# Performance work log

Measured on AMD Instinct MI355X. Metric: run time of the kernel, lower is better.

The kernel has to match this reference:

```python
import jax, jax.numpy as jnp
import numpy as np

DIM = 256; HEADS = 8; WSIZES = (8, 16); SHIFTS = (4, 8); H = 64; W = 64
NG = len(WSIZES)          # n_group
CH = DIM // NG            # channel per group = 128
GH = HEADS // NG          # gnum_heads = 4
GC = CH // GH             # gchannel (head dim) = 32
M = NG; D_SK = CH // 2    # SKConv: M groups, d = channel//r (r=2)


def _rel_pos_index(ws):
    coords = np.stack(np.meshgrid(np.arange(ws), np.arange(ws), indexing='ij'))
    cf = coords.reshape(2, -1)
    rel = (cf[:, :, None] - cf[:, None, :]).transpose(1, 2, 0).copy()
    rel[:, :, 0] += ws - 1
    rel[:, :, 1] += ws - 1
    rel[:, :, 0] *= 2 * ws - 1
    return rel.sum(-1)  # (ws*ws, ws*ws) int


def _attn_mask(ws, shift, Hp, Wp):
    img = np.zeros((Hp, Wp))
    sl = (slice(0, -ws), slice(-ws, -shift), slice(-shift, None))
    cnt = 0
    for hs in sl:
        for wsl in sl:
            img[hs, wsl] = cnt; cnt += 1
    mw = img.reshape(Hp // ws, ws, Wp // ws, ws).transpose(0, 2, 1, 3).reshape(-1, ws * ws)
    am = mw[:, None, :] - mw[:, :, None]  # unsqueeze(1) - unsqueeze(2)
    return np.where(am != 0, -100.0, 0.0).astype(np.float32)  # (nW, N, N)


def _part(x, ws):  # (B,H,W,C) -> (B*nW, ws, ws, C)
    B, Hx, Wx, C = x.shape
    x = x.reshape(B, Hx // ws, ws, Wx // ws, ws, C).transpose(0, 1, 3, 2, 4, 5)
    return x.reshape(-1, ws, ws, C)


def _reverse(win, ws, Hx, Wx, B):  # (B*nW, ws, ws, C) -> (B,H,W,C)
    C = win.shape[-1]
    x = win.reshape(B, Hx // ws, Wx // ws, ws, ws, C).transpose(0, 1, 3, 2, 4, 5)
    return x.reshape(B, Hx, Wx, C)


def _gelu(x):
    return jax.nn.gelu(x, approximate=False)  # torch nn.GELU default


def _skconv(x, pw, pb, f1w, f1b, f2w, f2b, phw, phb):
    bs, Hx, Wx, _ = x.shape
    # split channels into M groups of CH
    input_groups = x.transpose(0, 3, 1, 2).reshape(bs, M, CH, Hx, Wx)
    feats = x.reshape(bs, Hx * Wx, DIM) @ pw + pb
    feats_proj = feats.transpose(0, 2, 1).reshape(bs, DIM, Hx, Wx)
    fa = _gelu(feats).transpose(0, 2, 1).reshape(bs, DIM, Hx, Wx)
    feats_S = fa.mean(axis=(2, 3))                       # GAP -> (bs, DIM)
    z = _gelu(feats_S @ f1w + f1b)                       # (bs, d)
    av = (z @ f2w + f2b).reshape(bs, M, CH, 1, 1)
    av = jax.nn.softmax(av, axis=1)
    feats_V = (input_groups * av).sum(axis=1)            # (bs, CH, H, W)
    feats_V = feats_V.reshape(bs, CH, Hx * Wx).transpose(0, 2, 1) @ phw + phb
    feats_V = feats_V.transpose(0, 2, 1).reshape(bs, DIM, Hx, Wx)
    return feats_proj + feats_V


def _forward(x_q, x_kv, w_q, b_q, w_kv, b_kv, rpb0, rpb1,
             sk_proj_w, sk_proj_b, sk_fc1_w, sk_fc1_b, sk_fc2_w, sk_fc2_b,
             sk_head_w, sk_head_b):
    B = x_q.shape[0]
    q = (x_q.reshape(B, -1, DIM) @ w_q + b_q).reshape(B, H, W, DIM)
    kv = x_kv.reshape(B, -1, DIM) @ w_kv + b_kv           # (B, HW, 2*DIM)
    k = kv[..., :DIM].reshape(B, H, W, DIM)
    v = kv[..., DIM:].reshape(B, H, W, DIM)
    rpbs = (rpb0, rpb1)
    outs = []
    for i, (ws, sh) in enumerate(zip(WSIZES, SHIFTS)):
        qg = q[..., i * CH:(i + 1) * CH]
        kg = k[..., i * CH:(i + 1) * CH]
        vg = v[..., i * CH:(i + 1) * CH]
        if sh > 0:
            qg = jnp.roll(qg, (-sh, -sh), (1, 2))
            kg = jnp.roll(kg, (-sh, -sh), (1, 2))
            vg = jnp.roll(vg, (-sh, -sh), (1, 2))
        N = ws * ws
        qw = _part(qg, ws).reshape(-1, N, GH, GC).transpose(0, 2, 1, 3)  # (B_,GH,N,GC)
        kw = _part(kg, ws).reshape(-1, N, GH, GC).transpose(0, 2, 1, 3)
        vw = _part(vg, ws).reshape(-1, N, GH, GC).transpose(0, 2, 1, 3)
        scale = GC ** -0.5
        attn = jnp.einsum('bhnd,bhmd->bhnm', qw * scale, kw)
        idx = _rel_pos_index(ws).reshape(-1)
        bias = rpbs[i][idx].reshape(N, N, GH).transpose(2, 0, 1)         # (GH,N,N)
        attn = attn + bias[None]
        if sh > 0:
            mask = jnp.asarray(_attn_mask(ws, sh, H, W))                 # (nW,N,N)
            nW = mask.shape[0]
            attn = attn.reshape(-1, nW, GH, N, N) + mask[None, :, None]
            attn = attn.reshape(-1, GH, N, N)
        attn = jax.nn.softmax(attn, axis=-1)
        xw = jnp.einsum('bhnm,bhmd->bhnd', attn, vw)
        xw = xw.transpose(0, 2, 1, 3).reshape(-1, ws, ws, CH)
        xg = _reverse(xw, ws, H, W, B)
        if sh > 0:
            xg = jnp.roll(xg, (sh, sh), (1, 2))
        outs.append(xg)
    x = jnp.concatenate(outs, axis=-1)                    # (B,H,W,DIM)
    return _skconv(x, sk_proj_w, sk_proj_b, sk_fc1_w, sk_fc1_b,
                   sk_fc2_w, sk_fc2_b, sk_head_w, sk_head_b)


def setup_inputs() -> dict:
    key = jax.random.key(0)
    ks = jax.random.split(key, 16)
    B = 16
    s = lambda n: 1.0 / np.sqrt(n)
    return {
        'x_q': jax.random.normal(ks[0], (B, H, W, DIM), jnp.float32),
        'x_kv': jax.random.normal(ks[1], (B, H, W, DIM), jnp.float32),
        'w_q': jax.random.normal(ks[2], (DIM, DIM), jnp.float32) * s(DIM),
        'b_q': jnp.zeros((DIM,), jnp.float32),
        'w_kv': jax.random.normal(ks[3], (DIM, 2 * DIM), jnp.float32) * s(DIM),
        'b_kv': jnp.zeros((2 * DIM,), jnp.float32),
        'rpb0': jax.random.normal(ks[4], ((2 * WSIZES[0] - 1) ** 2, GH), jnp.float32) * 0.02,
        'rpb1': jax.random.normal(ks[5], ((2 * WSIZES[1] - 1) ** 2, GH), jnp.float32) * 0.02,
        'sk_proj_w': jax.random.normal(ks[6], (DIM, DIM), jnp.float32) * s(DIM),
        'sk_proj_b': jnp.zeros((DIM,), jnp.float32),
        'sk_fc1_w': jax.random.normal(ks[7], (DIM, D_SK), jnp.float32) * s(DIM),
        'sk_fc1_b': jnp.zeros((D_SK,), jnp.float32),
        'sk_fc2_w': jax.random.normal(ks[8], (D_SK, M * CH), jnp.float32) * s(D_SK),
        'sk_fc2_b': jnp.zeros((M * CH,), jnp.float32),
        'sk_head_w': jax.random.normal(ks[9], (CH, DIM), jnp.float32) * s(CH),
        'sk_head_b': jnp.zeros((DIM,), jnp.float32),
    }


def reference(x_q, x_kv, w_q, b_q, w_kv, b_kv, rpb0, rpb1,
              sk_proj_w, sk_proj_b, sk_fc1_w, sk_fc1_b, sk_fc2_w, sk_fc2_b,
              sk_head_w, sk_head_b):
    return _forward(x_q, x_kv, w_q, b_q, w_kv, b_kv, rpb0, rpb1,
                    sk_proj_w, sk_proj_b, sk_fc1_w, sk_fc1_b, sk_fc2_w, sk_fc2_b,
                    sk_head_w, sk_head_b)
```

## Files before the change

### kernel.cpp

```cpp
#include <hip/hip_runtime.h>
#include <cstddef>
#include <cstdint>


typedef __attribute__((ext_vector_type(8))) short short8v;
typedef __attribute__((ext_vector_type(4))) short short4v;
typedef __attribute__((ext_vector_type(4))) float f32x4;

__device__ __forceinline__ float gelu_f(float x) {
  return 0.5f * x * (1.0f + erff(x * 0.7071067811865475f));
}

__device__ __forceinline__ unsigned short f32_to_bf16_rne(float f) {
  unsigned u = __float_as_uint(f);
  unsigned r = 0x7FFFu + ((u >> 16) & 1u);
  return (unsigned short)((u + r) >> 16);
}
__device__ __forceinline__ float bf16_hi_to_f32(unsigned short h) {
  return __uint_as_float(((unsigned)h) << 16);
}

__global__ void decomp_w(const float* __restrict__ W,
                         unsigned short* __restrict__ hiT,
                         unsigned short* __restrict__ loT, int N, int K)
{
  const int k = blockIdx.y;
  const int n = blockIdx.x * 64 + threadIdx.x;
  const float f = W[(size_t)k * N + n];
  const unsigned short h = f32_to_bf16_rne(f);
  const unsigned short l = f32_to_bf16_rne(f - bf16_hi_to_f32(h));
  hiT[(size_t)n * K + k] = h;
  loT[(size_t)n * K + k] = l;
}

__global__ __launch_bounds__(512) void gemm_mfma_bias(
    const float* __restrict__ A, const unsigned short* __restrict__ WhT,
    const unsigned short* __restrict__ WlT, const float* __restrict__ bias,
    float* __restrict__ C, int N)
{
  constexpr int K = 256;
  __shared__ alignas(16) unsigned short Ah[4096];
  __shared__ alignas(16) unsigned short Al[4096];
  __shared__ alignas(16) unsigned short Bh[8192];
  __shared__ alignas(16) unsigned short Bl[8192];

  const int row0 = blockIdx.x * 128;
  const int col0 = blockIdx.y * 256;
  const int tid = threadIdx.x;
  const int lane = tid & 63;
  const int wave = tid >> 6;
  const int wm = wave >> 2, wn = wave & 3;

  f32x4 acc[4][4];
#pragma unroll
  for (int mi = 0; mi < 4; ++mi)
#pragma unroll
    for (int ni = 0; ni < 4; ++ni) {
      f32x4 z = {0.f, 0.f, 0.f, 0.f};
      acc[mi][ni] = z;
    }

  float4 pa[2];
  short8v pbh[2], pbl[2];

#define LOAD_TILE_QKV(k0_)                                                     \
  {                                                                            \
    _Pragma("unroll") for (int p = 0; p < 2; ++p) {                            \
      int flat = p * 512 + tid;                                                \
      int m = flat >> 3, kq = flat & 7;                                        \
      pa[p] = *(const float4*)(A + (size_t)(row0 + m) * K + (k0_) + kq * 4);   \
    }                                                                          \
    _Pragma("unroll") for (int p = 0; p < 2; ++p) {                            \
      int flat = p * 512 + tid;                                                \
      int n = flat >> 2, ko = flat & 3;                                        \
      const size_t off = (size_t)(col0 + n) * 256 + (k0_) + ko * 8;            \
      pbh[p] = *(const short8v*)(WhT + off);                                   \
      pbl[p] = *(const short8v*)(WlT + off);                                   \
    }                                                                          \
  }

  LOAD_TILE_QKV(0);

  for (int ks = 0; ks < 8; ++ks) {
    __syncthreads();
#pragma unroll
    for (int p = 0; p < 2; ++p) {
      int flat = p * 512 + tid;
      int m = flat >> 3, kq = flat & 7;
      float fx[4] = {pa[p].x, pa[p].y, pa[p].z, pa[p].w};
      unsigned short h[4], l[4];
#pragma unroll
      for (int j = 0; j < 4; ++j) {
        h[j] = f32_to_bf16_rne(fx[j]);
        l[j] = f32_to_bf16_rne(fx[j] - bf16_hi_to_f32(h[j]));
      }
      int e4 = (m >> 4) * 512 + (kq >> 1) * 128 + (m & 15) * 8 + (kq & 1) * 4;
      short4v hv = {(short)h[0], (short)h[1], (short)h[2], (short)h[3]};
      short4v lv = {(short)l[0], (short)l[1], (short)l[2], (short)l[3]};
      *(short4v*)&Ah[e4] = hv;
      *(short4v*)&Al[e4] = lv;
    }
#pragma unroll
    for (int p = 0; p < 2; ++p) {
      int flat = p * 512 + tid;
      int n = flat >> 2, ko = flat & 3;
      int e = (n >> 4) * 512 + ko * 128 + (n & 15) * 8;
      *(short8v*)&Bh[e] = pbh[p];
      *(short8v*)&Bl[e] = pbl[p];
    }
    __syncthreads();

    if (ks < 7) LOAD_TILE_QKV((ks + 1) * 32);

    short8v ah[4], alo[4], bh[4], blo[4];
#pragma unroll
    for (int mi = 0; mi < 4; ++mi) {
      int base = (wm * 4 + mi) * 512 + lane * 8;
      ah[mi] = *(const short8v*)&Ah[base];
      alo[mi] = *(const short8v*)&Al[base];
    }
#pragma unroll
    for (int ni = 0; ni < 4; ++ni) {
      int base = (wn * 4 + ni) * 512 + lane * 8;
      bh[ni] = *(const short8v*)&Bh[base];
      blo[ni] = *(const short8v*)&Bl[base];
    }
#pragma unroll
    for (int mi = 0; mi < 4; ++mi)
#pragma unroll
      for (int ni = 0; ni < 4; ++ni) {
        acc[mi][ni] = __builtin_amdgcn_mfma_f32_16x16x32_bf16(ah[mi], bh[ni], acc[mi][ni], 0, 0, 0);
        acc[mi][ni] = __builtin_amdgcn_mfma_f32_16x16x32_bf16(ah[mi], blo[ni], acc[mi][ni], 0, 0, 0);
        acc[mi][ni] = __builtin_amdgcn_mfma_f32_16x16x32_bf16(alo[mi], bh[ni], acc[mi][ni], 0, 0, 0);
      }
  }
#undef LOAD_TILE_QKV

#pragma unroll
  for (int mi = 0; mi < 4; ++mi) {
    const int rowb = row0 + wm * 64 + mi * 16 + (lane >> 4) * 4;
#pragma unroll
    for (int ni = 0; ni < 4; ++ni) {
      const int col = col0 + wn * 64 + ni * 16 + (lane & 15);
      const float bv = bias[col];
#pragma unroll
      for (int r = 0; r < 4; ++r)
        C[(size_t)(rowb + r) * N + col] = acc[mi][ni][r] + bv;
    }
  }
}

__global__ __launch_bounds__(512) void gemm_mfma_proj(
    const float* __restrict__ Act, const unsigned short* __restrict__ WhT,
    const unsigned short* __restrict__ WlT, const float* __restrict__ bias,
    float* __restrict__ featsT, float* __restrict__ part)
{
  __shared__ alignas(16) unsigned short Wh[4096];
  __shared__ alignas(16) unsigned short Wl[4096];
  __shared__ alignas(16) unsigned short Bh[8192];
  __shared__ alignas(16) unsigned short Bl[8192];
  __shared__ float pgelu[4][128];

  const int hw0 = blockIdx.x * 256;
  const int c0 = blockIdx.y * 128;
  const int b = hw0 >> 12;
  const int hwp0 = hw0 & 4095;
  const int tid = threadIdx.x;
  const int lane = tid & 63;
  const int wave = tid >> 6;
  const int wc = wave >> 2, wh = wave & 3;

  f32x4 acc[4][4];
#pragma unroll
  for (int mi = 0; mi < 4; ++mi)
#pragma unroll
    for (int ni = 0; ni < 4; ++ni) {
      f32x4 z = {0.f, 0.f, 0.f, 0.f};
      acc[mi][ni] = z;
    }

  float4 pact[4];
  short8v pwh, pwl;

#define LOAD_TILE_PROJ(k0_)                                                    \
  {                                                                            \
    _Pragma("unroll") for (int p = 0; p < 4; ++p) {                            \
      int f = p * 512 + tid;                                                   \
      int h = f >> 3, kq = f & 7;                                              \
      pact[p] = *(const float4*)(Act + (size_t)(hw0 + h) * 256 + (k0_) + kq * 4); \
    }                                                                          \
    {                                                                          \
      int c = tid >> 2, ko = tid & 3;                                          \
      const size_t off = (size_t)(c0 + c) * 256 + (k0_) + ko * 8;              \
      pwh = *(const short8v*)(WhT + off);                                      \
      pwl = *(const short8v*)(WlT + off);                                      \
    }                                                                          \
  }

  LOAD_TILE_PROJ(0);

  for (int ks = 0; ks < 8; ++ks) {
    __syncthreads();
    {
      int c = tid >> 2, ko = tid & 3;
      int e = (c >> 4) * 512 + ko * 128 + (c & 15) * 8;
      *(short8v*)&Wh[e] = pwh;
      *(short8v*)&Wl[e] = pwl;
    }
#pragma unroll
    for (int p = 0; p < 4; ++p) {
      int f = p * 512 + tid;
      int h = f >> 3, kq = f & 7;
      float fx[4] = {pact[p].x, pact[p].y, pact[p].z, pact[p].w};
      unsigned short hh[4], ll[4];
#pragma unroll
      for (int j = 0; j < 4; ++j) {
        hh[j] = f32_to_bf16_rne(fx[j]);
        ll[j] = f32_to_bf16_rne(fx[j] - bf16_hi_to_f32(hh[j]));
      }
      int e4 = (h >> 4) * 512 + (kq >> 1) * 128 + (h & 15) * 8 + (kq & 1) * 4;
      short4v hv = {(short)hh[0], (short)hh[1], (short)hh[2], (short)hh[3]};
      short4v lv = {(short)ll[0], (short)ll[1], (short)ll[2], (short)ll[3]};
      *(short4v*)&Bh[e4] = hv;
      *(short4v*)&Bl[e4] = lv;
    }
    __syncthreads();

    if (ks < 7) LOAD_TILE_PROJ((ks + 1) * 32);

    short8v wfh[4], wfl[4], bfh[4], bfl[4];
#pragma unroll
    for (int mi = 0; mi < 4; ++mi) {
      int base = (wc * 4 + mi) * 512 + lane * 8;
      wfh[mi] = *(const short8v*)&Wh[base];
      wfl[mi] = *(const short8v*)&Wl[base];
    }
#pragma unroll
    for (int ni = 0; ni < 4; ++ni) {
      int base = (wh * 4 + ni) * 512 + lane * 8;
      bfh[ni] = *(const short8v*)&Bh[base];
      bfl[ni] = *(const short8v*)&Bl[base];
    }
#pragma unroll
    for (int mi = 0; mi < 4; ++mi)
#pragma unroll
      for (int ni = 0; ni < 4; ++ni) {
        acc[mi][ni] = __builtin_amdgcn_mfma_f32_16x16x32_bf16(wfh[mi], bfh[ni], acc[mi][ni], 0, 0, 0);
        acc[mi][ni] = __builtin_amdgcn_mfma_f32_16x16x32_bf16(wfh[mi], bfl[ni], acc[mi][ni], 0, 0, 0);
        acc[mi][ni] = __builtin_amdgcn_mfma_f32_16x16x32_bf16(wfl[mi], bfh[ni], acc[mi][ni], 0, 0, 0);
      }
  }
#undef LOAD_TILE_PROJ

  float gsum[4][4];
#pragma unroll
  for (int mi = 0; mi < 4; ++mi)
#pragma unroll
    for (int r = 0; r < 4; ++r) gsum[mi][r] = 0.f;

#pragma unroll
  for (int mi = 0; mi < 4; ++mi) {
    const int c = c0 + wc * 64 + mi * 16 + (lane >> 4) * 4;
#pragma unroll
    for (int ni = 0; ni < 4; ++ni) {
      const int hwl = wh * 64 + ni * 16 + (lane & 15);
      const size_t base = ((size_t)b * 256 + c) * 4096 + hwp0 + hwl;
#pragma unroll
      for (int r = 0; r < 4; ++r) {
        const float val = acc[mi][ni][r] + bias[c + r];
        featsT[base + (size_t)r * 4096] = val;
        gsum[mi][r] += gelu_f(val);
      }
    }
  }
#pragma unroll
  for (int mi = 0; mi < 4; ++mi)
#pragma unroll
    for (int r = 0; r < 4; ++r) {
      float s = gsum[mi][r];
      s += __shfl_xor(s, 1);
      s += __shfl_xor(s, 2);
      s += __shfl_xor(s, 4);
      s += __shfl_xor(s, 8);
      gsum[mi][r] = s;
    }
  if ((lane & 15) == 0) {
#pragma unroll
    for (int mi = 0; mi < 4; ++mi)
#pragma unroll
      for (int r = 0; r < 4; ++r)
        pgelu[wh][wc * 64 + mi * 16 + (lane >> 4) * 4 + r] = gsum[mi][r];
  }
  __syncthreads();
  if (tid < 128) {
    const float s = pgelu[0][tid] + pgelu[1][tid] + pgelu[2][tid] + pgelu[3][tid];
    const int rbl = hwp0 >> 8;
    part[((size_t)b * 16 + rbl) * 256 + c0 + tid] = s;
  }
}

__global__ __launch_bounds__(512) void gemm_mfma_final(
    const float* __restrict__ Act, const float* __restrict__ featsT,
    const float* __restrict__ av, const unsigned short* __restrict__ WhT,
    const unsigned short* __restrict__ WlT, const float* __restrict__ bias,
    float* __restrict__ out)
{
  __shared__ alignas(16) unsigned short Wh[4096];
  __shared__ alignas(16) unsigned short Wl[4096];
  __shared__ alignas(16) unsigned short Bh[8192];
  __shared__ alignas(16) unsigned short Bl[8192];
  __shared__ float avs[256];

  const int hw0 = blockIdx.x * 256;
  const int c0 = blockIdx.y * 128;
  const int b = hw0 >> 12;
  const int hwp0 = hw0 & 4095;
  const int tid = threadIdx.x;
  const int lane = tid & 63;
  const int wave = tid >> 6;
  const int wc = wave >> 2, wh = wave & 3;

  if (tid < 256) avs[tid] = av[b * 256 + tid];

  f32x4 acc[4][4];
#pragma unroll
  for (int mi = 0; mi < 4; ++mi)
#pragma unroll
    for (int ni = 0; ni < 4; ++ni) {
      f32x4 z = {0.f, 0.f, 0.f, 0.f};
      acc[mi][ni] = z;
    }

  float4 px[4], py[4];
  short8v pwh, pwl;

#define LOAD_TILE_FIN(k0_)                                                     \
  {                                                                            \
    _Pragma("unroll") for (int p = 0; p < 4; ++p) {                            \
      int f = p * 512 + tid;                                                   \
      int h = f >> 3, kq = f & 7;                                              \
      const float* bp = Act + (size_t)(hw0 + h) * 256 + (k0_) + kq * 4;        \
      px[p] = *(const float4*)bp;                                              \
      py[p] = *(const float4*)(bp + 128);                                      \
    }                                                                          \
    {                                                                          \
      int c = tid >> 2, ko = tid & 3;                                          \
      const size_t off = (size_t)(c0 + c) * 128 + (k0_) + ko * 8;              \
      pwh = *(const short8v*)(WhT + off);                                      \
      pwl = *(const short8v*)(WlT + off);                                      \
    }                                                                          \
  }

  LOAD_TILE_FIN(0);

  for (int ks = 0; ks < 4; ++ks) {
    const int k0 = ks * 32;
    __syncthreads();
    {
      int c = tid >> 2, ko = tid & 3;
      int e = (c >> 4) * 512 + ko * 128 + (c & 15) * 8;
      *(short8v*)&Wh[e] = pwh;
      *(short8v*)&Wl[e] = pwl;
    }
#pragma unroll
    for (int p = 0; p < 4; ++p) {
      int f = p * 512 + tid;
      int h = f >> 3, kq = f & 7;
      const float4 a0 = *(const float4*)(avs + k0 + kq * 4);
      const float4 a1 = *(const float4*)(avs + 128 + k0 + kq * 4);
      float fx[4];
      fx[0] = px[p].x * a0.x + py[p].x * a1.x;
      fx[1] = px[p].y * a0.y + py[p].y * a1.y;
      fx[2] = px[p].z * a0.z + py[p].z * a1.z;
      fx[3] = px[p].w * a0.w + py[p].w * a1.w;
      unsigned short hh[4], ll[4];
#pragma unroll
      for (int j = 0; j < 4; ++j) {
        hh[j] = f32_to_bf16_rne(fx[j]);
        ll[j] = f32_to_bf16_rne(fx[j] - bf16_hi_to_f32(hh[j]));
      }
      int e4 = (h >> 4) * 512 + (kq >> 1) * 128 + (h & 15) * 8 + (kq & 1) * 4;
      short4v hv = {(short)hh[0], (short)hh[1], (short)hh[2], (short)hh[3]};
      short4v lv = {(short)ll[0], (short)ll[1], (short)ll[2], (short)ll[3]};
      *(short4v*)&Bh[e4] = hv;
      *(short4v*)&Bl[e4] = lv;
    }
    __syncthreads();

    if (ks < 3) LOAD_TILE_FIN((ks + 1) * 32);

    short8v wfh[4], wfl[4], bfh[4], bfl[4];
#pragma unroll
    for (int mi = 0; mi < 4; ++mi) {
      int base = (wc * 4 + mi) * 512 + lane * 8;
      wfh[mi] = *(const short8v*)&Wh[base];
      wfl[mi] = *(const short8v*)&Wl[base];
    }
#pragma unroll
    for (int ni = 0; ni < 4; ++ni) {
      int base = (wh * 4 + ni) * 512 + lane * 8;
      bfh[ni] = *(const short8v*)&Bh[base];
      bfl[ni] = *(const short8v*)&Bl[base];
    }
#pragma unroll
    for (int mi = 0; mi < 4; ++mi)
#pragma unroll
      for (int ni = 0; ni < 4; ++ni) {
        acc[mi][ni] = __builtin_amdgcn_mfma_f32_16x16x32_bf16(wfh[mi], bfh[ni], acc[mi][ni], 0, 0, 0);
        acc[mi][ni] = __builtin_amdgcn_mfma_f32_16x16x32_bf16(wfh[mi], bfl[ni], acc[mi][ni], 0, 0, 0);
        acc[mi][ni] = __builtin_amdgcn_mfma_f32_16x16x32_bf16(wfl[mi], bfh[ni], acc[mi][ni], 0, 0, 0);
      }
  }
#undef LOAD_TILE_FIN

#pragma unroll
  for (int mi = 0; mi < 4; ++mi) {
    const int c = c0 + wc * 64 + mi * 16 + (lane >> 4) * 4;
#pragma unroll
    for (int ni = 0; ni < 4; ++ni) {
      const int hwl = wh * 64 + ni * 16 + (lane & 15);
      const size_t base = ((size_t)b * 256 + c) * 4096 + hwp0 + hwl;
#pragma unroll
      for (int r = 0; r < 4; ++r)
        out[base + (size_t)r * 4096] =
            acc[mi][ni][r] + bias[c + r] + featsT[base + (size_t)r * 4096];
    }
  }
}

template <int WS, int SH, int GRP>
__global__ __launch_bounds__(WS * WS) void attn_kernel(
    float* qio, const float* __restrict__ kvbuf, const float* __restrict__ rpb)
{
  constexpr int N = WS * WS;
  constexpr int NW = 64 / WS;
  constexpr int NBIAS = (2 * WS - 1) * (2 * WS - 1);
  constexpr int LOGWS = (WS == 8) ? 3 : 4;

  __shared__ float ks[N][36];
  __shared__ float vs[N][36];
  __shared__ float sbias[NBIAS];
  __shared__ int sreg[N];

  const int head = blockIdx.x & 3;
  const int win = blockIdx.x >> 2;
  const int b = win / (NW * NW);
  const int wl = win % (NW * NW);
  const int wi = wl / NW, wj = wl % NW;
  const int t = threadIdx.x;
  const int ti = t >> LOGWS, tj = t & (WS - 1);
  const int hr = wi * WS + ti, wr = wj * WS + tj;
  const int hg = (hr + SH) & 63, wg = (wr + SH) & 63;
  const int cb = GRP * 128 + head * 32;

  const size_t pos = ((size_t)b * 64 + hg) * 64 + wg;
  float* qp = qio + pos * 256 + cb;
  const float* kp = kvbuf + pos * 512 + cb;
  const float* vp = kp + 256;

  constexpr float scale = 0.17677669529663687f;
  float qreg[32];
#pragma unroll
  for (int d4 = 0; d4 < 8; ++d4) {
    float4 qv = *(const float4*)(qp + d4 * 4);
    qreg[d4 * 4 + 0] = qv.x * scale; qreg[d4 * 4 + 1] = qv.y * scale;
    qreg[d4 * 4 + 2] = qv.z * scale; qreg[d4 * 4 + 3] = qv.w * scale;
    float4 kk4 = *(const float4*)(kp + d4 * 4);
    ks[t][d4 * 4 + 0] = kk4.x; ks[t][d4 * 4 + 1] = kk4.y;
    ks[t][d4 * 4 + 2] = kk4.z; ks[t][d4 * 4 + 3] = kk4.w;
    float4 vv4 = *(const float4*)(vp + d4 * 4);
    vs[t][d4 * 4 + 0] = vv4.x; vs[t][d4 * 4 + 1] = vv4.y;
    vs[t][d4 * 4 + 2] = vv4.z; vs[t][d4 * 4 + 3] = vv4.w;
  }
  for (int i = t; i < NBIAS; i += N) sbias[i] = rpb[i * 4 + head];
  const int rrh = (hr < 64 - WS) ? 0 : ((hr < 64 - SH) ? 1 : 2);
  const int rrw = (wr < 64 - WS) ? 0 : ((wr < 64 - SH) ? 1 : 2);
  const int myreg = rrh * 3 + rrw;
  sreg[t] = myreg;
  __syncthreads();

  float oacc[32];
#pragma unroll
  for (int d = 0; d < 32; ++d) oacc[d] = 0.f;
  float mrun = -1e30f, lrun = 0.f;
  const int tbias = (ti + WS - 1) * (2 * WS - 1) + (tj + WS - 1);

  for (int mc = 0; mc < N; mc += 32) {
    float s[32];
#pragma unroll
    for (int mm = 0; mm < 32; ++mm) {
      const int m = mc + mm;
      const float* kr = &ks[m][0];
      float dot = 0.f;
#pragma unroll
      for (int d4 = 0; d4 < 8; ++d4) {
        float4 k4 = *(const float4*)(kr + d4 * 4);
        dot += qreg[d4 * 4 + 0] * k4.x + qreg[d4 * 4 + 1] * k4.y +
               qreg[d4 * 4 + 2] * k4.z + qreg[d4 * 4 + 3] * k4.w;
      }
      const int mi = m >> LOGWS, mj = m & (WS - 1);
      float bias = sbias[tbias - mi * (2 * WS - 1) - mj];
      float msk = (sreg[m] == myreg) ? 0.f : -100.f;
      s[mm] = dot + bias + msk;
    }
    float mx = mrun;
#pragma unroll
    for (int mm = 0; mm < 32; ++mm) mx = fmaxf(mx, s[mm]);
    const float corr = expf(mrun - mx);
    lrun *= corr;
#pragma unroll
    for (int d = 0; d < 32; ++d) oacc[d] *= corr;
#pragma unroll
    for (int mm = 0; mm < 32; ++mm) {
      const int m = mc + mm;
      const float p = expf(s[mm] - mx);
      lrun += p;
      const float* vr = &vs[m][0];
#pragma unroll
      for (int d4 = 0; d4 < 8; ++d4) {
        float4 v4 = *(const float4*)(vr + d4 * 4);
        oacc[d4 * 4 + 0] += p * v4.x; oacc[d4 * 4 + 1] += p * v4.y;
        oacc[d4 * 4 + 2] += p * v4.z; oacc[d4 * 4 + 3] += p * v4.w;
      }
    }
    mrun = mx;
  }

  const float inv = 1.f / lrun;
#pragma unroll
  for (int d4 = 0; d4 < 8; ++d4) {
    float4 o;
    o.x = oacc[d4 * 4 + 0] * inv; o.y = oacc[d4 * 4 + 1] * inv;
    o.z = oacc[d4 * 4 + 2] * inv; o.w = oacc[d4 * 4 + 3] * inv;
    *(float4*)(qp + d4 * 4) = o;
  }
}

__global__ __launch_bounds__(256) void sk_small(
    const float* __restrict__ part, const float* __restrict__ f1w,
    const float* __restrict__ f1b, const float* __restrict__ f2w,
    const float* __restrict__ f2b, float* __restrict__ av)
{
  const int b = blockIdx.x;
  __shared__ float S[256];
  __shared__ float Z[64];
  __shared__ float Araw[256];
  const int tid = threadIdx.x;
  {
    float s = 0.f;
    for (int rb = 0; rb < 16; ++rb) s += part[((size_t)b * 16 + rb) * 256 + tid];
    S[tid] = s * (1.f / 4096.f);
  }
  __syncthreads();
  if (tid < 64) {
    float s = f1b[tid];
    for (int c = 0; c < 256; ++c) s += S[c] * f1w[c * 64 + tid];
    Z[tid] = gelu_f(s);
  }
  __syncthreads();
  {
    float s = f2b[tid];
    for (int j = 0; j < 64; ++j) s += Z[j] * f2w[j * 256 + tid];
    Araw[tid] = s;
  }
  __syncthreads();
  if (tid < 128) {
    float a0 = Araw[tid], a1 = Araw[128 + tid];
    float mx = fmaxf(a0, a1);
    float e0 = expf(a0 - mx), e1 = expf(a1 - mx);
    float inv = 1.f / (e0 + e1);
    av[b * 256 + tid] = e0 * inv;
    av[b * 256 + 128 + tid] = e1 * inv;
  }
}

extern "C" void kernel_launch(void* const* d_in, const int* in_sizes, int n_in,
                              void* d_out, int out_size, void* d_ws, size_t ws_size,
                              hipStream_t stream)
{
  (void)in_sizes; (void)n_in; (void)out_size;
  const float* x_q   = (const float*)d_in[0];
  const float* x_kv  = (const float*)d_in[1];
  const float* w_q   = (const float*)d_in[2];
  const float* b_q   = (const float*)d_in[3];
  const float* w_kv  = (const float*)d_in[4];
  const float* b_kv  = (const float*)d_in[5];
  const float* rpb0  = (const float*)d_in[6];
  const float* rpb1  = (const float*)d_in[7];
  const float* pw    = (const float*)d_in[8];
  const float* pb    = (const float*)d_in[9];
  const float* f1w   = (const float*)d_in[10];
  const float* f1b   = (const float*)d_in[11];
  const float* f2w   = (const float*)d_in[12];
  const float* f2b   = (const float*)d_in[13];
  const float* phw   = (const float*)d_in[14];
  const float* phb   = (const float*)d_in[15];
  float* out = (float*)d_out;

  float* ws = (float*)d_ws;
  float* qb  = ws;
  float* kvb = ws + 16777216;
  float* featsT = kvb;
  float* xatt = qb;

  const size_t tail_bytes = 1179648;
  uintptr_t tail_addr = ((uintptr_t)d_ws + ws_size - tail_bytes) & ~(uintptr_t)255;
  unsigned short* wqh = (unsigned short*)tail_addr;
  unsigned short* wql = wqh + 65536;
  unsigned short* wkh = wql + 65536;
  unsigned short* wkl = wkh + 131072;
  float* part = (float*)tail_addr;
  float* avb  = part + 65536;
  unsigned short* pwh = wkl + 131072;
  unsigned short* pwl = pwh + 65536;
  unsigned short* phh = pwl + 65536;
  unsigned short* phl = phh + 32768;

  decomp_w<<<dim3(4, 256), 64, 0, stream>>>(w_q, wqh, wql, 256, 256);
  decomp_w<<<dim3(8, 256), 64, 0, stream>>>(w_kv, wkh, wkl, 512, 256);
  decomp_w<<<dim3(4, 256), 64, 0, stream>>>(pw, pwh, pwl, 256, 256);
  decomp_w<<<dim3(4, 128), 64, 0, stream>>>(phw, phh, phl, 256, 128);
  gemm_mfma_bias<<<dim3(512, 1), 512, 0, stream>>>(x_q, wqh, wql, b_q, qb, 256);
  gemm_mfma_bias<<<dim3(512, 2), 512, 0, stream>>>(x_kv, wkh, wkl, b_kv, kvb, 512);
  attn_kernel<8, 4, 0><<<4096, 64, 0, stream>>>(qb, kvb, rpb0);
  attn_kernel<16, 8, 1><<<1024, 256, 0, stream>>>(qb, kvb, rpb1);
  gemm_mfma_proj<<<dim3(256, 2), 512, 0, stream>>>(xatt, pwh, pwl, pb, featsT, part);
  sk_small<<<16, 256, 0, stream>>>(part, f1w, f1b, f2w, f2b, avb);
  gemm_mfma_final<<<dim3(256, 2), 512, 0, stream>>>(xatt, featsT, avb, phh, phl, phb, out);
}
```

Baseline: 749.5 us.

## Stream K/V in quarter chunks to shrink attention LDS and raise occupancy

The window attention kernel now loads K and V into shared memory in four chunks of N/4 rows instead of the whole window at once. This cuts LDS use per block so more blocks can be resident, and the launch bounds now request four. The relative position bias is stored as bf16 and the region ids as bytes to shrink LDS further, and expf is swapped for __expf. In exchange the kernel adds extra barriers per chunk, loses some precision in the bias values, and keeps a serial load-then-compute pattern.

```diff
diff --git a/kernel.cpp b/kernel.cpp
--- a/kernel.cpp
+++ b/kernel.cpp
@@ -429,18 +429,20 @@
 }
 
 template <int WS, int SH, int GRP>
-__global__ __launch_bounds__(WS * WS) void attn_kernel(
+__global__ __launch_bounds__(WS * WS, 4) void attn_kernel(
     float* qio, const float* __restrict__ kvbuf, const float* __restrict__ rpb)
 {
   constexpr int N = WS * WS;
+  constexpr int CHUNK = N / 4;
+  constexpr int SUB = (CHUNK < 32) ? CHUNK : 32;
   constexpr int NW = 64 / WS;
   constexpr int NBIAS = (2 * WS - 1) * (2 * WS - 1);
   constexpr int LOGWS = (WS == 8) ? 3 : 4;
 
-  __shared__ float ks[N][36];
-  __shared__ float vs[N][36];
-  __shared__ float sbias[NBIAS];
-  __shared__ int sreg[N];
+  __shared__ float ks[CHUNK][36];
+  __shared__ float vs[CHUNK][36];
+  __shared__ unsigned short sbias[NBIAS];
+  __shared__ unsigned char sreg[N];
 
   const int head = blockIdx.x & 3;
   const int win = blockIdx.x >> 2;
@@ -455,8 +457,6 @@
 
   const size_t pos = ((size_t)b * 64 + hg) * 64 + wg;
   float* qp = qio + pos * 256 + cb;
-  const float* kp = kvbuf + pos * 512 + cb;
-  const float* vp = kp + 256;
 
   constexpr float scale = 0.17677669529663687f;
   float qreg[32];
@@ -465,19 +465,12 @@
     float4 qv = *(const float4*)(qp + d4 * 4);
     qreg[d4 * 4 + 0] = qv.x * scale; qreg[d4 * 4 + 1] = qv.y * scale;
     qreg[d4 * 4 + 2] = qv.z * scale; qreg[d4 * 4 + 3] = qv.w * scale;
-    float4 kk4 = *(const float4*)(kp + d4 * 4);
-    ks[t][d4 * 4 + 0] = kk4.x; ks[t][d4 * 4 + 1] = kk4.y;
-    ks[t][d4 * 4 + 2] = kk4.z; ks[t][d4 * 4 + 3] = kk4.w;
-    float4 vv4 = *(const float4*)(vp + d4 * 4);
-    vs[t][d4 * 4 + 0] = vv4.x; vs[t][d4 * 4 + 1] = vv4.y;
-    vs[t][d4 * 4 + 2] = vv4.z; vs[t][d4 * 4 + 3] = vv4.w;
-  }
-  for (int i = t; i < NBIAS; i += N) sbias[i] = rpb[i * 4 + head];
+  }
+  for (int i = t; i < NBIAS; i += N) sbias[i] = f32_to_bf16_rne(rpb[i * 4 + head]);
   const int rrh = (hr < 64 - WS) ? 0 : ((hr < 64 - SH) ? 1 : 2);
   const int rrw = (wr < 64 - WS) ? 0 : ((wr < 64 - SH) ? 1 : 2);
   const int myreg = rrh * 3 + rrw;
-  sreg[t] = myreg;
-  __syncthreads();
+  sreg[t] = (unsigned char)myreg;
 
   float oacc[32];
 #pragma unroll
@@ -485,45 +478,68 @@
   float mrun = -1e30f, lrun = 0.f;
   const int tbias = (ti + WS - 1) * (2 * WS - 1) + (tj + WS - 1);
 
-  for (int mc = 0; mc < N; mc += 32) {
-    float s[32];
-#pragma unroll
-    for (int mm = 0; mm < 32; ++mm) {
-      const int m = mc + mm;
-      const float* kr = &ks[m][0];
-      float dot = 0.f;
-#pragma unroll
-      for (int d4 = 0; d4 < 8; ++d4) {
-        float4 k4 = *(const float4*)(kr + d4 * 4);
-        dot += qreg[d4 * 4 + 0] * k4.x + qreg[d4 * 4 + 1] * k4.y +
-               qreg[d4 * 4 + 2] * k4.z + qreg[d4 * 4 + 3] * k4.w;
-      }
-      const int mi = m >> LOGWS, mj = m & (WS - 1);
-      float bias = sbias[tbias - mi * (2 * WS - 1) - mj];
-      float msk = (sreg[m] == myreg) ? 0.f : -100.f;
-      s[mm] = dot + bias + msk;
-    }
-    float mx = mrun;
-#pragma unroll
-    for (int mm = 0; mm < 32; ++mm) mx = fmaxf(mx, s[mm]);
-    const float corr = expf(mrun - mx);
-    lrun *= corr;
-#pragma unroll
-    for (int d = 0; d < 32; ++d) oacc[d] *= corr;
-#pragma unroll
-    for (int mm = 0; mm < 32; ++mm) {
-      const int m = mc + mm;
-      const float p = expf(s[mm] - mx);
-      lrun += p;
-      const float* vr = &vs[m][0];
-#pragma unroll
-      for (int d4 = 0; d4 < 8; ++d4) {
-        float4 v4 = *(const float4*)(vr + d4 * 4);
-        oacc[d4 * 4 + 0] += p * v4.x; oacc[d4 * 4 + 1] += p * v4.y;
-        oacc[d4 * 4 + 2] += p * v4.z; oacc[d4 * 4 + 3] += p * v4.w;
-      }
-    }
-    mrun = mx;
+  for (int c = 0; c < 4; ++c) {
+    __syncthreads();
+    {
+      const int rl = t >> 2;
+      const int qc = t & 3;
+      const int m = c * CHUNK + rl;
+      const int kmi = m >> LOGWS, kmj = m & (WS - 1);
+      const int hk = (wi * WS + kmi + SH) & 63;
+      const int wk = (wj * WS + kmj + SH) & 63;
+      const float* kpm =
+          kvbuf + (((size_t)b * 64 + hk) * 64 + wk) * 512 + cb + qc * 8;
+      const float* vpm = kpm + 256;
+#pragma unroll
+      for (int d4 = 0; d4 < 2; ++d4) {
+        *(float4*)&ks[rl][qc * 8 + d4 * 4] = *(const float4*)(kpm + d4 * 4);
+        *(float4*)&vs[rl][qc * 8 + d4 * 4] = *(const float4*)(vpm + d4 * 4);
+      }
+    }
+    __syncthreads();
+
+    for (int mc = 0; mc < CHUNK; mc += SUB) {
+      float s[SUB];
+#pragma unroll
+      for (int mm = 0; mm < SUB; ++mm) {
+        const int ml = mc + mm;
+        const int mg = c * CHUNK + ml;
+        const float* kr = &ks[ml][0];
+        float dot = 0.f;
+#pragma unroll
+        for (int d4 = 0; d4 < 8; ++d4) {
+          float4 k4 = *(const float4*)(kr + d4 * 4);
+          dot += qreg[d4 * 4 + 0] * k4.x + qreg[d4 * 4 + 1] * k4.y +
+                 qreg[d4 * 4 + 2] * k4.z + qreg[d4 * 4 + 3] * k4.w;
+        }
+        const int kmi = mg >> LOGWS, kmj = mg & (WS - 1);
+        const float bias =
+            bf16_hi_to_f32(sbias[tbias - kmi * (2 * WS - 1) - kmj]);
+        const float msk = (sreg[mg] == myreg) ? 0.f : -100.f;
+        s[mm] = dot + bias + msk;
+      }
+      float mx = mrun;
+#pragma unroll
+      for (int mm = 0; mm < SUB; ++mm) mx = fmaxf(mx, s[mm]);
+      const float corr = __expf(mrun - mx);
+      lrun *= corr;
+#pragma unroll
+      for (int d = 0; d < 32; ++d) oacc[d] *= corr;
+#pragma unroll
+      for (int mm = 0; mm < SUB; ++mm) {
+        const int ml = mc + mm;
+        const float p = __expf(s[mm] - mx);
+        lrun += p;
+        const float* vr = &vs[ml][0];
+#pragma unroll
+        for (int d4 = 0; d4 < 8; ++d4) {
+          float4 v4 = *(const float4*)(vr + d4 * 4);
+          oacc[d4 * 4 + 0] += p * v4.x; oacc[d4 * 4 + 1] += p * v4.y;
+          oacc[d4 * 4 + 2] += p * v4.z; oacc[d4 * 4 + 3] += p * v4.w;
+        }
+      }
+      mrun = mx;
+    }
   }
 
   const float inv = 1.f / lrun;
```

Result: faster. 708.4 us (-5.5%).
